# Kernel optimization log

Hardware: AMD Instinct MI355X
Metric: run time of the kernel (lower is better)

Reference implementation:

```python
import jax, jax.numpy as jnp
import numpy as np
from functools import partial

CHANNEL_N = 16
FIRE_RATE = 0.5
SCALE_GROWTH = 1.0
SCALE_GROWTH_SYNTH = 1.0
ANGLE = 0.0


def _sobel_kernels(angle, channel_n):
    # dx = outer([1,2,1],[-1,0,1])/8 ; dy = dx.T ; rotated by angle (degrees)
    dx = np.outer([1.0, 2.0, 1.0], [-1.0, 0.0, 1.0]) / 8.0
    dy = dx.T
    c, s = np.cos(angle * np.pi / 180.0), np.sin(angle * np.pi / 180.0)
    w1 = (c * dx - s * dy).astype(np.float32)
    w2 = (s * dx + c * dy).astype(np.float32)
    # depthwise conv weights, OIHW with O=channel_n, I=1 (groups=channel_n)
    k1 = jnp.asarray(np.tile(w1[None, None], (channel_n, 1, 1, 1)))
    k2 = jnp.asarray(np.tile(w2[None, None], (channel_n, 1, 1, 1)))
    return k1, k2


def _depthwise(x_nchw, k):
    return jax.lax.conv_general_dilated(
        x_nchw, k, window_strides=(1, 1), padding=((1, 1), (1, 1)),
        dimension_numbers=('NCHW', 'OIHW', 'NCHW'),
        feature_group_count=x_nchw.shape[1])


def _alive(x_nchw):
    # 3x3 max-pool (stride 1, pad 1) on channel 1, threshold 0.1
    a = x_nchw[:, 1:2]
    m = jax.lax.reduce_window(a, -jnp.inf, jax.lax.max,
                              (1, 1, 3, 3), (1, 1, 1, 1),
                              ((0, 0), (0, 0), (1, 1), (1, 1)))
    return m > 0.1


def _update(x, w0, b0, w1, key):
    # x: [B,H,W,C]; torch does x.transpose(1,3) -> [B,C,W,H]
    xt = jnp.transpose(x, (0, 3, 2, 1))
    pre_life = _alive(xt)
    k1, k2 = _sobel_kernels(ANGLE, xt.shape[1])
    y = jnp.concatenate([xt, _depthwise(xt, k1), _depthwise(xt, k2)], axis=1)  # [B,3C,W,H]
    d = jnp.transpose(y, (0, 3, 2, 1))  # [B,H,W,3C]
    h = jax.nn.relu(jnp.einsum('bhwc,cd->bhwd', d, w0) + b0)
    dx = jnp.einsum('bhwd,dc->bhwc', h, w1)
    stoch = (jax.random.uniform(key, dx.shape[:3] + (1,)) > FIRE_RATE).astype(dx.dtype)
    dx = dx * stoch * (SCALE_GROWTH * SCALE_GROWTH_SYNTH)
    xt = xt + jnp.transpose(dx, (0, 3, 2, 1))
    post_life = _alive(xt)
    xt = xt * (pre_life & post_life).astype(xt.dtype)
    return jnp.transpose(xt, (0, 3, 2, 1))


def setup_inputs() -> dict:
    key = jax.random.key(0)
    k1, k2, k3, k4 = jax.random.split(key, 4)
    B, H, W, C, HID = 16, 256, 256, CHANNEL_N, 128
    x = jax.random.uniform(k1, (B, H, W, C), dtype=jnp.float32)
    w0 = jax.random.normal(k2, (3 * C, HID), dtype=jnp.float32) * 0.05
    b0 = jax.random.normal(k3, (HID,), dtype=jnp.float32) * 0.05
    w1 = jax.random.normal(k4, (HID, C), dtype=jnp.float32) * 0.05
    return {'x': x, 'w0': w0, 'b0': b0, 'w1': w1, 'steps': 1}


def reference(x, w0, b0, w1, steps):
    key = jax.random.key(42)
    for step in range(steps):
        x = _update(x, w0, b0, w1, jax.random.fold_in(key, step))
    return x
```

## Files before the change

kernel.cpp:

```cpp
#include <hip/hip_runtime.h>
#include <hip/hip_bf16.h>

#define BB 16
#define HH 256
#define WW 256
#define CC 16
#define HID 128
#define NPIX (BB*HH*WW)
#define NBLK (BB*HH)

#define PCL_STRIDE 36
#define PCL_WAVE   (64*PCL_STRIDE)
#define W0T_STRIDE 52

typedef __attribute__((ext_vector_type(8))) short s16x8;
typedef __attribute__((ext_vector_type(4))) float f32x4;

union V8 { uint4 u; uint2 h[2]; s16x8 s; };

struct Key2 { unsigned a, b; };

__host__ __device__ constexpr unsigned rotl32c(unsigned x, int d) {
    return (x << d) | (x >> (32 - d));
}

__host__ __device__ constexpr Key2 tf2x32(unsigned k0, unsigned k1, unsigned x0, unsigned x1) {
    const unsigned ks2 = k0 ^ k1 ^ 0x1BD11BDAu;
    const int R[5][4] = {{13,15,26,6},{17,29,16,24},{13,15,26,6},{17,29,16,24},{13,15,26,6}};
    const unsigned ka[5] = {k1, ks2, k0, k1, ks2};
    const unsigned kb[5] = {ks2, k0, k1, ks2, k0};
    x0 += k0; x1 += k1;
    for (int i = 0; i < 5; ++i) {
        for (int j = 0; j < 4; ++j) { x0 += x1; x1 = rotl32c(x1, R[i][j]); x1 ^= x0; }
        x0 += ka[i] + (unsigned)0; x1 += kb[i] + (unsigned)(i + 1);
    }
    return Key2{x0, x1};
}
constexpr Key2 FK = tf2x32(0u, 42u, 0u, 0u);

__device__ inline unsigned pk2(float a, float b) {
    union { __hip_bfloat162 h2; unsigned u; } cv;
    cv.h2 = __float22bfloat162_rn(make_float2(a, b));
    return cv.u;
}

__global__ __launch_bounds__(256, 4)
void ca_fused(const float* __restrict__ x, const float* __restrict__ w0,
              const float* __restrict__ b0, const float* __restrict__ w1,
              float* __restrict__ out, float* __restrict__ ch1new,
              unsigned char* __restrict__ prelife)
{
    __shared__ short percL[4 * PCL_WAVE];
    __shared__ short w0T[128 * W0T_STRIDE];

    const int tid = threadIdx.x;
    const unsigned bid = blockIdx.x;
    const unsigned lb = (bid & 7u) * 512u + (bid >> 3);
    const int h = lb & 255, b = lb >> 8;
    const unsigned jbase = lb << 8;
    const unsigned j = jbase + tid;
    const int wave = tid >> 6, lane = tid & 63;
    const int l15 = lane & 15, g = lane >> 4;

    {
        const int n = tid & 127, half = tid >> 7;
        float v[24];
        #pragma unroll
        for (int kk = 0; kk < 24; ++kk) v[kk] = w0[(half * 24 + kk) * HID + n];
        #pragma unroll
        for (int c = 0; c < 6; ++c) {
            uint2 pkv;
            pkv.x = pk2(v[c*4+0], v[c*4+1]);
            pkv.y = pk2(v[c*4+2], v[c*4+3]);
            *reinterpret_cast<uint2*>(&w0T[n * W0T_STRIDE + half * 24 + c * 4]) = pkv;
        }
    }

    float conv[32];
    #pragma unroll
    for (int i = 0; i < 32; ++i) conv[i] = 0.0f;
    float maxc1 = -3.0e38f;
    const float vt[3] = {1.0f, 2.0f, 1.0f};
    const float ut[3] = {-1.0f, 0.0f, 1.0f};
    #pragma unroll
    for (int dh = -1; dh <= 1; ++dh) {
        #pragma unroll
        for (int dw = -1; dw <= 1; ++dw) {
            const int h2 = h + dh, w2 = tid + dw;
            if ((unsigned)h2 < HH && (unsigned)w2 < WW) {
                const float* p = x + ((((size_t)b * HH + h2) * WW + w2) * CC);
                const float c1 = vt[dw + 1] * ut[dh + 1] * 0.125f;
                const float c2 = ut[dw + 1] * vt[dh + 1] * 0.125f;
                #pragma unroll
                for (int q = 0; q < 4; ++q) {
                    const float4 v4 = *reinterpret_cast<const float4*>(p + q * 4);
                    if (dh != 0) {
                        conv[q*4+0] = fmaf(c1, v4.x, conv[q*4+0]);
                        conv[q*4+1] = fmaf(c1, v4.y, conv[q*4+1]);
                        conv[q*4+2] = fmaf(c1, v4.z, conv[q*4+2]);
                        conv[q*4+3] = fmaf(c1, v4.w, conv[q*4+3]);
                    }
                    if (dw != 0) {
                        conv[16+q*4+0] = fmaf(c2, v4.x, conv[16+q*4+0]);
                        conv[16+q*4+1] = fmaf(c2, v4.y, conv[16+q*4+1]);
                        conv[16+q*4+2] = fmaf(c2, v4.z, conv[16+q*4+2]);
                        conv[16+q*4+3] = fmaf(c2, v4.w, conv[16+q*4+3]);
                    }
                    if (q == 0 && dh == 0 && dw == 0) maxc1 = fmaxf(maxc1, v4.y);
                    else if (q == 0) maxc1 = fmaxf(maxc1, v4.y);
                }
            }
        }
    }

    {
        const int base = wave * PCL_WAVE + lane * PCL_STRIDE;
        #pragma unroll
        for (int c = 0; c < 8; ++c) {
            uint2 pkv;
            pkv.x = pk2(conv[c*4 + 0], conv[c*4 + 1]);
            pkv.y = pk2(conv[c*4 + 2], conv[c*4 + 3]);
            *reinterpret_cast<uint2*>(&percL[base + c * 4]) = pkv;
        }
    }

    const Key2 r = tf2x32(FK.a, FK.b, 0u, j);
    const unsigned bits = r.a ^ r.b;
    const float uu = __uint_as_float((bits >> 9) | 0x3f800000u) - 1.0f;
    const unsigned long long kmask = __ballot(uu > 0.5f);
    prelife[j] = (maxc1 > 0.1f) ? (unsigned char)1 : (unsigned char)0;

    __syncthreads();

    const unsigned pixbase = jbase + wave * 64;
    s16x8 pB0[4], pB1[4];
    #pragma unroll
    for (int mt = 0; mt < 4; ++mt) {
        const int prow = wave * PCL_WAVE + (mt * 16 + l15) * PCL_STRIDE;
        V8 f0, f1;
        if (g < 2) {
            const float* xp = &x[(size_t)(pixbase + mt * 16 + l15) * CC + g * 8];
            const float4 va = *reinterpret_cast<const float4*>(xp);
            const float4 vb = *reinterpret_cast<const float4*>(xp + 4);
            f0.u.x = pk2(va.x, va.y); f0.u.y = pk2(va.z, va.w);
            f0.u.z = pk2(vb.x, vb.y); f0.u.w = pk2(vb.z, vb.w);
            f1.h[0] = *reinterpret_cast<const uint2*>(&percL[prow + 16 + g * 8]);
            f1.h[1] = *reinterpret_cast<const uint2*>(&percL[prow + 16 + g * 8 + 4]);
        } else {
            f0.h[0] = *reinterpret_cast<const uint2*>(&percL[prow + (g - 2) * 8]);
            f0.h[1] = *reinterpret_cast<const uint2*>(&percL[prow + (g - 2) * 8 + 4]);
            f1.u = make_uint4(0u, 0u, 0u, 0u);
        }
        pB0[mt] = f0.s;
        pB1[mt] = f1.s;
    }

    __builtin_amdgcn_sched_barrier(0);

    short* HPw = &percL[wave * PCL_WAVE];
    f32x4 acc2[4];
    #pragma unroll
    for (int mt2 = 0; mt2 < 4; ++mt2) acc2[mt2] = 0.0f;

    #pragma unroll
    for (int p = 0; p < 4; ++p) {
        s16x8 w0f0[2], w0f1[2];
        #pragma unroll
        for (int nt = 0; nt < 2; ++nt) {
            const int n = p * 32 + nt * 16 + l15;
            V8 a0, a1;
            a0.h[0] = *reinterpret_cast<const uint2*>(&w0T[n * W0T_STRIDE + g * 8]);
            a0.h[1] = *reinterpret_cast<const uint2*>(&w0T[n * W0T_STRIDE + g * 8 + 4]);
            if (g < 2) {
                a1.h[0] = *reinterpret_cast<const uint2*>(&w0T[n * W0T_STRIDE + 32 + g * 8]);
                a1.h[1] = *reinterpret_cast<const uint2*>(&w0T[n * W0T_STRIDE + 32 + g * 8 + 4]);
            } else {
                a1.u = make_uint4(0u, 0u, 0u, 0u);
            }
            w0f0[nt] = a0.s; w0f1[nt] = a1.s;
        }
        #pragma unroll
        for (int mt = 0; mt < 4; ++mt) {
            #pragma unroll
            for (int nt = 0; nt < 2; ++nt) {
                const float4 bv = *reinterpret_cast<const float4*>(&b0[p*32 + nt*16 + g*4]);
                f32x4 acc = {bv.x, bv.y, bv.z, bv.w};
                acc = __builtin_amdgcn_mfma_f32_16x16x32_bf16(w0f0[nt], pB0[mt], acc, 0, 0, 0);
                acc = __builtin_amdgcn_mfma_f32_16x16x32_bf16(w0f1[nt], pB1[mt], acc, 0, 0, 0);
                uint2 hv;
                hv.x = pk2(fmaxf(acc[0], 0.f), fmaxf(acc[1], 0.f));
                hv.y = pk2(fmaxf(acc[2], 0.f), fmaxf(acc[3], 0.f));
                const int m = mt * 16 + l15;
                *reinterpret_cast<uint2*>(
                    &HPw[m * 32 + 4 * ((4*nt + g) ^ (l15 & 6))]) = hv;
            }
        }
        {
            float wv[8];
            #pragma unroll
            for (int e = 0; e < 8; ++e) wv[e] = w1[(p * 32 + g * 8 + e) * CC + l15];
            V8 wf;
            wf.u.x = pk2(wv[0], wv[1]); wf.u.y = pk2(wv[2], wv[3]);
            wf.u.z = pk2(wv[4], wv[5]); wf.u.w = pk2(wv[6], wv[7]);
            #pragma unroll
            for (int mt2 = 0; mt2 < 4; ++mt2) {
                const int m = mt2 * 16 + l15;
                const s16x8 hp = *reinterpret_cast<const s16x8*>(
                    &HPw[m * 32 + 4 * ((2*g) ^ (l15 & 6))]);
                acc2[mt2] = __builtin_amdgcn_mfma_f32_16x16x32_bf16(wf.s, hp, acc2[mt2], 0, 0, 0);
            }
        }
    }

    #pragma unroll
    for (int mt2 = 0; mt2 < 4; ++mt2) {
        const int prel = mt2 * 16 + l15;
        const unsigned pj = pixbase + prel;
        const float kv = ((kmask >> prel) & 1ull) ? 1.0f : 0.0f;
        const float4 x4 = *reinterpret_cast<const float4*>(&x[(size_t)pj * CC + g * 4]);
        float4 v;
        v.x = x4.x + acc2[mt2][0] * kv;
        v.y = x4.y + acc2[mt2][1] * kv;
        v.z = x4.z + acc2[mt2][2] * kv;
        v.w = x4.w + acc2[mt2][3] * kv;
        *reinterpret_cast<float4*>(&out[(size_t)pj * CC + g * 4]) = v;
        if (g == 0) ch1new[pj] = v.y;
    }
}

__global__ __launch_bounds__(256)
void ca_step2(float* __restrict__ out, const float* __restrict__ ch1new,
              const unsigned char* __restrict__ prelife)
{
    const int tid = threadIdx.x;
    const int lane = tid & 63;
    const int rowi = tid >> 6;
    const unsigned bid = blockIdx.x;
    const int hq = bid & 63, b = bid >> 6;
    const int h = hq * 4 + rowi;
    const unsigned rowbase = ((unsigned)(b * HH + h)) * WW;
    const int w0 = lane * 4;

    float4 vc = *reinterpret_cast<const float4*>(&ch1new[rowbase + w0]);
    float m0 = vc.x, m1 = vc.y, m2 = vc.z, m3 = vc.w;
    if (h > 0) {
        float4 vu = *reinterpret_cast<const float4*>(&ch1new[rowbase - WW + w0]);
        m0 = fmaxf(m0, vu.x); m1 = fmaxf(m1, vu.y); m2 = fmaxf(m2, vu.z); m3 = fmaxf(m3, vu.w);
    }
    if (h < HH - 1) {
        float4 vd = *reinterpret_cast<const float4*>(&ch1new[rowbase + WW + w0]);
        m0 = fmaxf(m0, vd.x); m1 = fmaxf(m1, vd.y); m2 = fmaxf(m2, vd.z); m3 = fmaxf(m3, vd.w);
    }
    float left  = __shfl_up(m3, 1);   if (lane == 0)  left  = -3.0e38f;
    float right = __shfl_down(m0, 1); if (lane == 63) right = -3.0e38f;

    float mm[4];
    mm[0] = fmaxf(fmaxf(left, m0), m1);
    mm[1] = fmaxf(fmaxf(m0, m1), m2);
    mm[2] = fmaxf(fmaxf(m1, m2), m3);
    mm[3] = fmaxf(fmaxf(m2, m3), right);

    const uchar4 pl = *reinterpret_cast<const uchar4*>(&prelife[rowbase + w0]);
    const unsigned char pla[4] = {pl.x, pl.y, pl.z, pl.w};
    #pragma unroll
    for (int i = 0; i < 4; ++i) {
        const bool alive = (pla[i] != 0) && (mm[i] > 0.1f);
        if (!alive) {
            const float4 z = make_float4(0.f, 0.f, 0.f, 0.f);
            float4* o = reinterpret_cast<float4*>(out + (size_t)(rowbase + w0 + i) * CC);
            o[0] = z; o[1] = z; o[2] = z; o[3] = z;
        }
    }
}

extern "C" void kernel_launch(void* const* d_in, const int* in_sizes, int n_in,
                              void* d_out, int out_size, void* d_ws, size_t ws_size,
                              hipStream_t stream) {
    const float* x  = (const float*)d_in[0];
    const float* w0 = (const float*)d_in[1];
    const float* b0 = (const float*)d_in[2];
    const float* w1 = (const float*)d_in[3];
    float* out = (float*)d_out;

    float* ch1new = (float*)d_ws;
    unsigned char* prelife = (unsigned char*)d_ws + (size_t)NPIX * 4;

    ca_fused<<<dim3(NBLK), dim3(256), 0, stream>>>(x, w0, b0, w1, out, ch1new, prelife);
    ca_step2<<<dim3(NPIX / 1024), dim3(256), 0, stream>>>(out, ch1new, prelife);
}
```

Before: 75.45 us.

## Pre-pack bf16 MFMA weight fragments in a prep kernel and drop per-block LDS staging

Adds a tiny single-block prep kernel that converts w0 and w1 to bf16 already laid out in per-lane MFMA fragment order in workspace. The main kernel now loads these fragments straight from global (cache-resident) memory instead of having every block transpose and convert w0 into shared memory and convert w1 in registers. This removes the per-block weight staging, its LDS footprint and a __syncthreads. The launch bound is raised from 4 to 8 blocks per CU, at the cost of one extra kernel launch.

```diff
diff --git a/kernel.cpp b/kernel.cpp
--- a/kernel.cpp
+++ b/kernel.cpp
@@ -11,7 +11,6 @@
 
 #define PCL_STRIDE 36
 #define PCL_WAVE   (64*PCL_STRIDE)
-#define W0T_STRIDE 52
 
 typedef __attribute__((ext_vector_type(8))) short s16x8;
 typedef __attribute__((ext_vector_type(4))) float f32x4;
@@ -32,7 +31,7 @@
     x0 += k0; x1 += k1;
     for (int i = 0; i < 5; ++i) {
         for (int j = 0; j < 4; ++j) { x0 += x1; x1 = rotl32c(x1, R[i][j]); x1 ^= x0; }
-        x0 += ka[i] + (unsigned)0; x1 += kb[i] + (unsigned)(i + 1);
+        x0 += ka[i]; x1 += kb[i] + (unsigned)(i + 1);
     }
     return Key2{x0, x1};
 }
@@ -44,14 +43,47 @@
     return cv.u;
 }
 
-__global__ __launch_bounds__(256, 4)
-void ca_fused(const float* __restrict__ x, const float* __restrict__ w0,
-              const float* __restrict__ b0, const float* __restrict__ w1,
+__global__ __launch_bounds__(256)
+void ca_prep(const float* __restrict__ w0, const float* __restrict__ w1,
+             short* __restrict__ w0bf, short* __restrict__ w1bf)
+{
+    const int t = threadIdx.x;
+    #pragma unroll
+    for (int rr = 0; rr < 4; ++rr) {
+        const int row = rr * 256 + t;
+        const int l15 = row & 15, g = (row >> 4) & 3, ks = (row >> 6) & 1;
+        const int nt = (row >> 7) & 1, p = row >> 8;
+        const int n = p * 32 + nt * 16 + l15;
+        float v[8];
+        #pragma unroll
+        for (int jj = 0; jj < 8; ++jj) {
+            const int kg = ks * 32 + g * 8 + jj;
+            v[jj] = (kg < 48) ? w0[kg * HID + n] : 0.0f;
+        }
+        uint4 pkv;
+        pkv.x = pk2(v[0], v[1]); pkv.y = pk2(v[2], v[3]);
+        pkv.z = pk2(v[4], v[5]); pkv.w = pk2(v[6], v[7]);
+        *reinterpret_cast<uint4*>(&w0bf[row * 8]) = pkv;
+    }
+    {
+        const int l15 = t & 15, g = (t >> 4) & 3, p = t >> 6;
+        float v[8];
+        #pragma unroll
+        for (int e = 0; e < 8; ++e) v[e] = w1[(p * 32 + g * 8 + e) * CC + l15];
+        uint4 pkv;
+        pkv.x = pk2(v[0], v[1]); pkv.y = pk2(v[2], v[3]);
+        pkv.z = pk2(v[4], v[5]); pkv.w = pk2(v[6], v[7]);
+        *reinterpret_cast<uint4*>(&w1bf[t * 8]) = pkv;
+    }
+}
+
+__global__ __launch_bounds__(256, 8)
+void ca_fused(const float* __restrict__ x, const short* __restrict__ w0bf,
+              const float* __restrict__ b0, const short* __restrict__ w1bf,
               float* __restrict__ out, float* __restrict__ ch1new,
               unsigned char* __restrict__ prelife)
 {
     __shared__ short percL[4 * PCL_WAVE];
-    __shared__ short w0T[128 * W0T_STRIDE];
 
     const int tid = threadIdx.x;
     const unsigned bid = blockIdx.x;
@@ -61,20 +93,6 @@
     const unsigned j = jbase + tid;
     const int wave = tid >> 6, lane = tid & 63;
     const int l15 = lane & 15, g = lane >> 4;
-
-    {
-        const int n = tid & 127, half = tid >> 7;
-        float v[24];
-        #pragma unroll
-        for (int kk = 0; kk < 24; ++kk) v[kk] = w0[(half * 24 + kk) * HID + n];
-        #pragma unroll
-        for (int c = 0; c < 6; ++c) {
-            uint2 pkv;
-            pkv.x = pk2(v[c*4+0], v[c*4+1]);
-            pkv.y = pk2(v[c*4+2], v[c*4+3]);
-            *reinterpret_cast<uint2*>(&w0T[n * W0T_STRIDE + half * 24 + c * 4]) = pkv;
-        }
-    }
 
     float conv[32];
     #pragma unroll
@@ -106,8 +124,7 @@
                         conv[16+q*4+2] = fmaf(c2, v4.z, conv[16+q*4+2]);
                         conv[16+q*4+3] = fmaf(c2, v4.w, conv[16+q*4+3]);
                     }
-                    if (q == 0 && dh == 0 && dw == 0) maxc1 = fmaxf(maxc1, v4.y);
-                    else if (q == 0) maxc1 = fmaxf(maxc1, v4.y);
+                    if (q == 0) maxc1 = fmaxf(maxc1, v4.y);
                 }
             }
         }
@@ -129,8 +146,6 @@
     const float uu = __uint_as_float((bits >> 9) | 0x3f800000u) - 1.0f;
     const unsigned long long kmask = __ballot(uu > 0.5f);
     prelife[j] = (maxc1 > 0.1f) ? (unsigned char)1 : (unsigned char)0;
-
-    __syncthreads();
 
     const unsigned pixbase = jbase + wave * 64;
     s16x8 pB0[4], pB1[4];
@@ -157,6 +172,9 @@
 
     __builtin_amdgcn_sched_barrier(0);
 
+    const s16x8* w0F = reinterpret_cast<const s16x8*>(w0bf);
+    const s16x8* w1F = reinterpret_cast<const s16x8*>(w1bf);
+
     short* HPw = &percL[wave * PCL_WAVE];
     f32x4 acc2[4];
     #pragma unroll
@@ -167,17 +185,8 @@
         s16x8 w0f0[2], w0f1[2];
         #pragma unroll
         for (int nt = 0; nt < 2; ++nt) {
-            const int n = p * 32 + nt * 16 + l15;
-            V8 a0, a1;
-            a0.h[0] = *reinterpret_cast<const uint2*>(&w0T[n * W0T_STRIDE + g * 8]);
-            a0.h[1] = *reinterpret_cast<const uint2*>(&w0T[n * W0T_STRIDE + g * 8 + 4]);
-            if (g < 2) {
-                a1.h[0] = *reinterpret_cast<const uint2*>(&w0T[n * W0T_STRIDE + 32 + g * 8]);
-                a1.h[1] = *reinterpret_cast<const uint2*>(&w0T[n * W0T_STRIDE + 32 + g * 8 + 4]);
-            } else {
-                a1.u = make_uint4(0u, 0u, 0u, 0u);
-            }
-            w0f0[nt] = a0.s; w0f1[nt] = a1.s;
+            w0f0[nt] = w0F[((p * 2 + nt) * 2 + 0) * 64 + lane];
+            w0f1[nt] = w0F[((p * 2 + nt) * 2 + 1) * 64 + lane];
         }
         #pragma unroll
         for (int mt = 0; mt < 4; ++mt) {
@@ -196,18 +205,13 @@
             }
         }
         {
-            float wv[8];
-            #pragma unroll
-            for (int e = 0; e < 8; ++e) wv[e] = w1[(p * 32 + g * 8 + e) * CC + l15];
-            V8 wf;
-            wf.u.x = pk2(wv[0], wv[1]); wf.u.y = pk2(wv[2], wv[3]);
-            wf.u.z = pk2(wv[4], wv[5]); wf.u.w = pk2(wv[6], wv[7]);
+            const s16x8 wf = w1F[p * 64 + lane];
             #pragma unroll
             for (int mt2 = 0; mt2 < 4; ++mt2) {
                 const int m = mt2 * 16 + l15;
                 const s16x8 hp = *reinterpret_cast<const s16x8*>(
                     &HPw[m * 32 + 4 * ((2*g) ^ (l15 & 6))]);
-                acc2[mt2] = __builtin_amdgcn_mfma_f32_16x16x32_bf16(wf.s, hp, acc2[mt2], 0, 0, 0);
+                acc2[mt2] = __builtin_amdgcn_mfma_f32_16x16x32_bf16(wf, hp, acc2[mt2], 0, 0, 0);
             }
         }
     }
@@ -284,7 +288,10 @@
 
     float* ch1new = (float*)d_ws;
     unsigned char* prelife = (unsigned char*)d_ws + (size_t)NPIX * 4;
-
-    ca_fused<<<dim3(NBLK), dim3(256), 0, stream>>>(x, w0, b0, w1, out, ch1new, prelife);
+    short* w0bf = (short*)((char*)d_ws + 5242880);
+    short* w1bf = (short*)((char*)d_ws + 5242880 + 16384);
+
+    ca_prep<<<dim3(1), dim3(256), 0, stream>>>(w0, w1, w0bf, w1bf);
+    ca_fused<<<dim3(NBLK), dim3(256), 0, stream>>>(x, w0bf, b0, w1bf, out, ch1new, prelife);
     ca_step2<<<dim3(NPIX / 1024), dim3(256), 0, stream>>>(out, ch1new, prelife);
 }
```

Result: slower. 206.3 us (+173.5%).
